# Performance work log

Measured on AMD Instinct MI355X. Metric: run time of the kernel, lower is better.

The kernel has to match this reference:

```python
import jax, jax.numpy as jnp
import numpy as np

B, N, FN, FE = 8, 256, 64, 64  # batch, nodes, node feat, edge feat


def gnn_layer(A, x, e, We, be, Wn, bn):
    # A: [B,N,N] float mask, x: [B,N,Fn], e: [B,N,N,Fe_in]
    b, n, fn = x.shape
    xi = jnp.broadcast_to(x[:, :, None, :], (b, n, n, fn))  # sender feats
    xj = jnp.broadcast_to(x[:, None, :, :], (b, n, n, fn))  # receiver feats
    h = jnp.concatenate([xi, xj, e], axis=-1)               # [B,N,N,2Fn+Fe]
    e_new = jax.nn.relu(jnp.einsum('bijk,kf->bijf', h, We) + be) * A[..., None]
    deg = jnp.clip(jnp.sum(A, axis=2), 1.0, None)           # [B,N]
    agg = jnp.sum(e_new, axis=2) / deg[..., None]           # mean over neighbors
    x_new = jax.nn.relu(jnp.concatenate([x, agg], axis=-1) @ Wn + bn)
    return x_new, e_new


def setup_inputs() -> dict:
    key = jax.random.key(0)
    ks = jax.random.split(key, 20)
    s = 0.05
    inp = {
        'edge_index': jax.random.randint(ks[0], (B, N, N), 0, 2, dtype=jnp.int32),
        'x': jax.random.normal(ks[1], (B, N, FN), dtype=jnp.float32),
        'edge_attr': jax.random.normal(ks[2], (B, N, N, FE), dtype=jnp.float32),
    }
    # 3 GNN layers: edge-update MLP (2Fn+Fe -> Fe) and node-update (Fn+Fe -> Fn)
    for l in range(3):
        inp[f'We{l}'] = jax.random.normal(ks[3 + 4 * l], (2 * FN + FE, FE), jnp.float32) * s
        inp[f'be{l}'] = jnp.zeros((FE,), jnp.float32)
        inp[f'Wn{l}'] = jax.random.normal(ks[4 + 4 * l], (FN + FE, FN), jnp.float32) * s
        inp[f'bn{l}'] = jnp.zeros((FN,), jnp.float32)
    # spectral-norm MLP head: Fe -> Fe -> Fe -> 1
    inp['W1'] = jax.random.normal(ks[15], (FE, FE), jnp.float32) * s
    inp['b1'] = jnp.zeros((FE,), jnp.float32)
    inp['W2'] = jax.random.normal(ks[16], (FE, FE), jnp.float32) * s
    inp['b2'] = jnp.zeros((FE,), jnp.float32)
    inp['W3'] = jax.random.normal(ks[17], (FE, 1), jnp.float32) * s
    inp['b3'] = jnp.zeros((1,), jnp.float32)
    return inp


def reference(edge_index, x, edge_attr,
              We0, be0, Wn0, bn0,
              We1, be1, Wn1, bn1,
              We2, be2, Wn2, bn2,
              W1, b1, W2, b2, W3, b3):
    A = edge_index.astype(jnp.float32)
    x = x.astype(jnp.float32)
    # layer 0 updates both nodes and edges
    x1, e = gnn_layer(A, x, edge_attr, We0, be0, Wn0, bn0)
    # middle layer(s): node output discarded (as in original forward)
    _, e = gnn_layer(A, x1, e, We1, be1, Wn1, bn1)
    # last layer
    _, edges = gnn_layer(A, x1, e, We2, be2, Wn2, bn2)
    # end == 'edge_mean'
    v = jnp.mean(edges, axis=(1, 2))  # [B, FE]
    h = jax.nn.relu(v @ W1 + b1)
    h = jax.nn.relu(h @ W2 + b2)
    out = h @ W3 + b3                  # [B, 1]
    return jnp.squeeze(out, axis=-1)   # [B]
```

## Files before the change

kernel.cpp:

```cpp
#include <hip/hip_runtime.h>

#define BB 8
#define NN 256
#define FF 64

typedef float f32x4 __attribute__((ext_vector_type(4)));
typedef short s16x8 __attribute__((ext_vector_type(8)));
typedef unsigned short u16;

#define MFMA_BF16(a, b, c) __builtin_amdgcn_mfma_f32_16x16x32_bf16(a, b, c, 0, 0, 0)

__device__ inline u16 f2bf(float x) {
    unsigned u = __float_as_uint(x);
    u += 0x7FFFu + ((u >> 16) & 1u);
    return (u16)(u >> 16);
}
__device__ inline float bf2f(u16 h) { return __uint_as_float(((unsigned)h) << 16); }

__device__ inline s16x8 cvt_a(float4 v0, float4 v1) {
    s16x8 a;
    a[0] = (short)f2bf(v0.x); a[1] = (short)f2bf(v0.y);
    a[2] = (short)f2bf(v0.z); a[3] = (short)f2bf(v0.w);
    a[4] = (short)f2bf(v1.x); a[5] = (short)f2bf(v1.y);
    a[6] = (short)f2bf(v1.z); a[7] = (short)f2bf(v1.w);
    return a;
}

__global__ __launch_bounds__(256) void wprep_kernel(
    const float* __restrict__ We0, const float* __restrict__ We1,
    const float* __restrict__ We2, u16* __restrict__ wimg)
{
    const float* src =
        (blockIdx.x == 0 ? We0 : (blockIdx.x == 1 ? We1 : We2)) + 2 * FF * FF;
    u16* hi = wimg + blockIdx.x * 8192;
    u16* lo = hi + 4096;
    for (int idx = threadIdx.x; idx < 4096; idx += 256) {
        const int f = idx >> 6, rem = idx & 63, cs = rem >> 3, j = rem & 7;
        const int k = ((cs ^ (f & 7)) << 3) | j;
        const float wv = src[k * FF + f];
        const u16 h = f2bf(wv);
        hi[idx] = h;
        lo[idx] = f2bf(wv - bf2f(h));
    }
}

__global__ __launch_bounds__(256) void pq_kernel(
    const float* __restrict__ x, const float* __restrict__ We,
    const float* __restrict__ be, float* __restrict__ P, float* __restrict__ QT,
    float* __restrict__ agg)
{
    const int rl = threadIdx.x >> 6, f = threadIdx.x & 63;
    const int r = blockIdx.x * 4 + rl;
    __shared__ float xs[4][FF];
    xs[rl][f] = x[r * FF + f];
    agg[r * FF + f] = 0.f;
    __syncthreads();
    float p = be[f], q = 0.f;
#pragma unroll
    for (int k = 0; k < FF; ++k) {
        const float xv = xs[rl][k];
        p = fmaf(xv, We[k * FF + f], p);
        q = fmaf(xv, We[(FF + k) * FF + f], q);
    }
    P[r * FF + f] = p;
    QT[((r >> 8) * FF + f) * NN + (r & 255)] = q;
}

__global__ __launch_bounds__(256, 4) void edge0_kernel(
    const float* e_in, const u16* __restrict__ whi,
    const u16* __restrict__ wlo, const float* __restrict__ P,
    const float* __restrict__ QT0, const int* __restrict__ A,
    u16* e1_out, float* __restrict__ agg)
{
    __shared__ u16 Whl[4096], Wll[4096];
    __shared__ u16 Et[8192];
    __shared__ float Al[128], Pl[64];

    const int tid = threadIdx.x;
    const int bt  = blockIdx.x;
    const int bi  = bt >> 1;
    const int b   = bi >> 8;
    const int j0  = (bt & 1) << 7;

#pragma unroll
    for (int m = 0; m < 2; ++m) {
        ((uint4*)Whl)[tid + 256 * m] = ((const uint4*)whi)[tid + 256 * m];
        ((uint4*)Wll)[tid + 256 * m] = ((const uint4*)wlo)[tid + 256 * m];
    }
    if (tid < 128) Al[tid] = (float)A[bi * NN + j0 + tid];
    if (tid < 64)  Pl[tid] = P[bi * FF + tid];

    const int w = tid >> 6, lane = tid & 63;
    const int quad = lane >> 4, l15 = lane & 15, l7 = lane & 7;
    const int e_base = 32 * w;

    const float* erow = e_in + ((size_t)bi * NN + j0) * FF;
    const int*   Arow = A + bi * NN + j0;

    int rm[2];
#pragma unroll
    for (int et = 0; et < 2; ++et) rm[et] = Arow[e_base + et * 16 + l15];

    float al[2][4];
#pragma unroll
    for (int et = 0; et < 2; ++et) {
        const int4 ai = *(const int4*)&Arow[e_base + et * 16 + quad * 4];
        al[et][0] = (float)ai.x; al[et][1] = (float)ai.y;
        al[et][2] = (float)ai.z; al[et][3] = (float)ai.w;
    }

    s16x8 afr[2][2];
#pragma unroll
    for (int et = 0; et < 2; ++et) {
        if (rm[et]) {
#pragma unroll
            for (int ks = 0; ks < 2; ++ks) {
                const float* p =
                    erow + (e_base + et * 16 + l15) * FF + ks * 32 + quad * 8;
                afr[ks][et] = cvt_a(*(const float4*)p, *(const float4*)(p + 4));
            }
        } else {
#pragma unroll
            for (int ks = 0; ks < 2; ++ks) afr[ks][et] = (s16x8){0,0,0,0,0,0,0,0};
        }
    }

    float qv[2][4][4];
    {
        const float* QTb = QT0 + (size_t)b * FF * NN;
#pragma unroll
        for (int et = 0; et < 2; ++et)
#pragma unroll
            for (int ft = 0; ft < 4; ++ft) {
                const float4 t = *(const float4*)
                    &QTb[(ft * 16 + l15) * NN + j0 + e_base + et * 16 + quad * 4];
                qv[et][ft][0] = t.x; qv[et][ft][1] = t.y;
                qv[et][ft][2] = t.z; qv[et][ft][3] = t.w;
            }
    }

    __syncthreads();

    f32x4 acc[2][4];
#pragma unroll
    for (int et = 0; et < 2; ++et)
#pragma unroll
        for (int ft = 0; ft < 4; ++ft) acc[et][ft] = (f32x4){0.f, 0.f, 0.f, 0.f};

#pragma unroll
    for (int ks = 0; ks < 2; ++ks)
#pragma unroll
        for (int ft = 0; ft < 4; ++ft) {
            const int f  = ft * 16 + l15;
            const int ca = (ks * 4 + quad) ^ l7;
            const s16x8 bh = *(const s16x8*)&Whl[f * 64 + ca * 8];
            const s16x8 bl = *(const s16x8*)&Wll[f * 64 + ca * 8];
#pragma unroll
            for (int et = 0; et < 2; ++et) {
                acc[et][ft] = MFMA_BF16(afr[ks][et], bh, acc[et][ft]);
                acc[et][ft] = MFMA_BF16(afr[ks][et], bl, acc[et][ft]);
            }
        }

    float psum[4] = {0.f, 0.f, 0.f, 0.f};
#pragma unroll
    for (int et = 0; et < 2; ++et)
#pragma unroll
        for (int ft = 0; ft < 4; ++ft)
#pragma unroll
            for (int r = 0; r < 4; ++r) {
                const int el = e_base + et * 16 + quad * 4 + r;
                const int f  = ft * 16 + l15;
                const float val = acc[et][ft][r] + Pl[f] + qv[et][ft][r];
                const float rv  = fmaxf(val, 0.f) * al[et][r];
                Et[el * 64 + f] = f2bf(rv);
                psum[ft] += rv;
            }
#pragma unroll
    for (int ft = 0; ft < 4; ++ft) {
        psum[ft] += __shfl_down(psum[ft], 32);
        psum[ft] += __shfl_down(psum[ft], 16);
    }
    if (lane < 16) {
#pragma unroll
        for (int ft = 0; ft < 4; ++ft)
            atomicAdd(&agg[bi * FF + ft * 16 + l15], psum[ft]);
    }

    __syncthreads();

    u16* dst = e1_out + (size_t)bt * 16384;
#pragma unroll
    for (int m = 0; m < 4; ++m) {
        const int idx = tid + 256 * m;
        const int row = idx >> 3;
        if (Al[row] != 0.f)
            ((uint4*)dst)[idx] = ((const uint4*)Et)[idx];
    }
}

__global__ __launch_bounds__(256) void nodepq_kernel(
    const float* __restrict__ x, const float* __restrict__ agg,
    const int* __restrict__ A,
    const float* __restrict__ Wn, const float* __restrict__ bn,
    const float* __restrict__ We1, const float* __restrict__ be1,
    const float* __restrict__ We2, const float* __restrict__ be2,
    float* __restrict__ P1, float* __restrict__ QT1,
    float* __restrict__ P2, float* __restrict__ QT2, float* __restrict__ v)
{
    const int rl = threadIdx.x >> 6, f = threadIdx.x & 63;
    const int r = blockIdx.x * 4 + rl;
    __shared__ float s[4][2 * FF];
    __shared__ float x1s[4][FF];

    float da = (float)A[r * NN + f] + (float)A[r * NN + f + 64] +
               (float)A[r * NN + f + 128] + (float)A[r * NN + f + 192];
#pragma unroll
    for (int off = 32; off > 0; off >>= 1) da += __shfl_down(da, off, 64);
    const float deg = fmaxf(__shfl(da, 0, 64), 1.0f);

    s[rl][f]      = x[r * FF + f];
    s[rl][FF + f] = agg[r * FF + f] / deg;
    if (blockIdx.x == 0) {
        v[threadIdx.x] = 0.f;
        v[256 + threadIdx.x] = 0.f;
    }
    __syncthreads();
    float a = bn[f];
#pragma unroll
    for (int k = 0; k < 2 * FF; ++k) a = fmaf(s[rl][k], Wn[k * FF + f], a);
    x1s[rl][f] = fmaxf(a, 0.f);
    __syncthreads();
    float p1 = be1[f], q1 = 0.f, p2 = be2[f], q2 = 0.f;
#pragma unroll
    for (int k = 0; k < FF; ++k) {
        const float xv = x1s[rl][k];
        p1 = fmaf(xv, We1[k * FF + f], p1);
        q1 = fmaf(xv, We1[(FF + k) * FF + f], q1);
        p2 = fmaf(xv, We2[k * FF + f], p2);
        q2 = fmaf(xv, We2[(FF + k) * FF + f], q2);
    }
    P1[r * FF + f] = p1;
    P2[r * FF + f] = p2;
    const int qt = ((r >> 8) * FF + f) * NN + (r & 255);
    QT1[qt] = q1;
    QT2[qt] = q2;
}

__global__ __launch_bounds__(256, 4) void edge12_kernel(
    const u16* __restrict__ e1,
    const u16* __restrict__ w1hi, const u16* __restrict__ w1lo,
    const u16* __restrict__ w2hi, const u16* __restrict__ w2lo,
    const float* __restrict__ P1, const float* __restrict__ QT1,
    const float* __restrict__ P2, const float* __restrict__ QT2,
    const int* __restrict__ A, float* __restrict__ v)
{
    __shared__ u16 Wh[4096], Wl[4096];
    __shared__ u16 E2[128 * 64];
    __shared__ float Pl1[64], Pl2[64], red[64];

    const int tid = threadIdx.x;
    const int bt  = blockIdx.x;
    const int bi  = bt >> 1;
    const int b   = bi >> 8;
    const int j0  = (bt & 1) << 7;

    const uint4 w2h0 = ((const uint4*)w2hi)[tid];
    const uint4 w2h1 = ((const uint4*)w2hi)[tid + 256];
    const uint4 w2l0 = ((const uint4*)w2lo)[tid];
    const uint4 w2l1 = ((const uint4*)w2lo)[tid + 256];

#pragma unroll
    for (int m = 0; m < 2; ++m) {
        ((uint4*)Wh)[tid + 256 * m] = ((const uint4*)w1hi)[tid + 256 * m];
        ((uint4*)Wl)[tid + 256 * m] = ((const uint4*)w1lo)[tid + 256 * m];
    }
    if (tid < 64) {
        Pl1[tid] = P1[bi * FF + tid];
        Pl2[tid] = P2[bi * FF + tid];
        red[tid] = 0.f;
    }

    const int w = tid >> 6, lane = tid & 63;
    const int quad = lane >> 4, l15 = lane & 15, l7 = lane & 7;
    const int e_base = 32 * w;

    const int* Arow = A + bi * NN + j0;

    int rm[2];
#pragma unroll
    for (int et = 0; et < 2; ++et) rm[et] = Arow[e_base + et * 16 + l15];

    float al[2][4];
#pragma unroll
    for (int et = 0; et < 2; ++et) {
        const int4 ai = *(const int4*)&Arow[e_base + et * 16 + quad * 4];
        al[et][0] = (float)ai.x; al[et][1] = (float)ai.y;
        al[et][2] = (float)ai.z; al[et][3] = (float)ai.w;
    }

    const u16* etile = e1 + (size_t)bt * 16384;
    s16x8 afr[2][2];
#pragma unroll
    for (int et = 0; et < 2; ++et) {
        if (rm[et]) {
#pragma unroll
            for (int ks = 0; ks < 2; ++ks)
                afr[ks][et] = *(const s16x8*)
                    &etile[(e_base + et * 16 + l15) * 64 + ks * 32 + quad * 8];
        } else {
#pragma unroll
            for (int ks = 0; ks < 2; ++ks) afr[ks][et] = (s16x8){0,0,0,0,0,0,0,0};
        }
    }

    float qv[2][4][4];
    {
        const float* QTb = QT1 + (size_t)b * FF * NN;
#pragma unroll
        for (int et = 0; et < 2; ++et)
#pragma unroll
            for (int ft = 0; ft < 4; ++ft) {
                const float4 t = *(const float4*)
                    &QTb[(ft * 16 + l15) * NN + j0 + e_base + et * 16 + quad * 4];
                qv[et][ft][0] = t.x; qv[et][ft][1] = t.y;
                qv[et][ft][2] = t.z; qv[et][ft][3] = t.w;
            }
    }

    __syncthreads();

    f32x4 acc[2][4];
#pragma unroll
    for (int et = 0; et < 2; ++et)
#pragma unroll
        for (int ft = 0; ft < 4; ++ft) acc[et][ft] = (f32x4){0.f, 0.f, 0.f, 0.f};

#pragma unroll
    for (int ks = 0; ks < 2; ++ks)
#pragma unroll
        for (int ft = 0; ft < 4; ++ft) {
            const int f  = ft * 16 + l15;
            const int ca = (ks * 4 + quad) ^ l7;
            const s16x8 bh = *(const s16x8*)&Wh[f * 64 + ca * 8];
            const s16x8 bl = *(const s16x8*)&Wl[f * 64 + ca * 8];
#pragma unroll
            for (int et = 0; et < 2; ++et) {
                acc[et][ft] = MFMA_BF16(afr[ks][et], bh, acc[et][ft]);
                acc[et][ft] = MFMA_BF16(afr[ks][et], bl, acc[et][ft]);
            }
        }

#pragma unroll
    for (int et = 0; et < 2; ++et)
#pragma unroll
        for (int ft = 0; ft < 4; ++ft)
#pragma unroll
            for (int r = 0; r < 4; ++r) {
                const int el = e_base + et * 16 + quad * 4 + r;
                const int f  = ft * 16 + l15;
                const float val = acc[et][ft][r] + Pl1[f] + qv[et][ft][r];
                const float rv  = fmaxf(val, 0.f) * al[et][r];
                const int c  = f >> 3;
                const int cs = c ^ (el & 7);
                E2[el * 64 + cs * 8 + l7] = f2bf(rv);
            }

    {
        const float* QTb = QT2 + (size_t)b * FF * NN;
#pragma unroll
        for (int et = 0; et < 2; ++et)
#pragma unroll
            for (int ft = 0; ft < 4; ++ft) {
                const float4 t = *(const float4*)
                    &QTb[(ft * 16 + l15) * NN + j0 + e_base + et * 16 + quad * 4];
                qv[et][ft][0] = t.x; qv[et][ft][1] = t.y;
                qv[et][ft][2] = t.z; qv[et][ft][3] = t.w;
            }
    }

    __syncthreads();

    ((uint4*)Wh)[tid]       = w2h0;
    ((uint4*)Wh)[tid + 256] = w2h1;
    ((uint4*)Wl)[tid]       = w2l0;
    ((uint4*)Wl)[tid + 256] = w2l1;

    __syncthreads();

#pragma unroll
    for (int et = 0; et < 2; ++et)
#pragma unroll
        for (int ft = 0; ft < 4; ++ft) acc[et][ft] = (f32x4){0.f, 0.f, 0.f, 0.f};

#pragma unroll
    for (int ks = 0; ks < 2; ++ks) {
        s16x8 a2[2];
#pragma unroll
        for (int et = 0; et < 2; ++et) {
            const int e  = e_base + et * 16 + l15;
            const int ca = (ks * 4 + quad) ^ l7;
            a2[et] = *(const s16x8*)&E2[e * 64 + ca * 8];
        }
#pragma unroll
        for (int ft = 0; ft < 4; ++ft) {
            const int f  = ft * 16 + l15;
            const int ca = (ks * 4 + quad) ^ l7;
            const s16x8 bh = *(const s16x8*)&Wh[f * 64 + ca * 8];
            const s16x8 bl = *(const s16x8*)&Wl[f * 64 + ca * 8];
#pragma unroll
            for (int et = 0; et < 2; ++et) {
                acc[et][ft] = MFMA_BF16(a2[et], bh, acc[et][ft]);
                acc[et][ft] = MFMA_BF16(a2[et], bl, acc[et][ft]);
            }
        }
    }

    float psum[4] = {0.f, 0.f, 0.f, 0.f};
#pragma unroll
    for (int et = 0; et < 2; ++et)
#pragma unroll
        for (int ft = 0; ft < 4; ++ft)
#pragma unroll
            for (int r = 0; r < 4; ++r) {
                const float val = acc[et][ft][r] + Pl2[ft * 16 + l15] + qv[et][ft][r];
                psum[ft] += fmaxf(val, 0.f) * al[et][r];
            }
#pragma unroll
    for (int ft = 0; ft < 4; ++ft) {
        psum[ft] += __shfl_down(psum[ft], 32);
        psum[ft] += __shfl_down(psum[ft], 16);
    }
    if (lane < 16) {
#pragma unroll
        for (int ft = 0; ft < 4; ++ft)
            atomicAdd(&red[ft * 16 + l15], psum[ft]);
    }
    __syncthreads();
    if (tid < 64) atomicAdd(&v[b * FF + tid], red[tid]);
}

__global__ __launch_bounds__(64) void head_kernel(
    const float* __restrict__ vsum, const float* __restrict__ W1,
    const float* __restrict__ b1, const float* __restrict__ W2,
    const float* __restrict__ b2, const float* __restrict__ W3,
    const float* __restrict__ b3, float* __restrict__ out)
{
    const int f = threadIdx.x;
    __shared__ float hv[BB][FF];
    __shared__ float h1[BB][FF];
#pragma unroll
    for (int b = 0; b < BB; ++b) hv[b][f] = vsum[b * FF + f] * (1.0f / 65536.0f);
    __syncthreads();
#pragma unroll
    for (int b = 0; b < BB; ++b) {
        float acc = b1[f];
#pragma unroll
        for (int k = 0; k < FF; ++k) acc = fmaf(hv[b][k], W1[k * FF + f], acc);
        h1[b][f] = fmaxf(acc, 0.f);
    }
    __syncthreads();
#pragma unroll
    for (int b = 0; b < BB; ++b) {
        float acc = b2[f];
#pragma unroll
        for (int k = 0; k < FF; ++k) acc = fmaf(h1[b][k], W2[k * FF + f], acc);
        hv[b][f] = fmaxf(acc, 0.f);
    }
    __syncthreads();
#pragma unroll
    for (int b = 0; b < BB; ++b) {
        float p = hv[b][f] * W3[f];
#pragma unroll
        for (int off = 32; off > 0; off >>= 1) p += __shfl_down(p, off);
        if (f == 0) out[b] = p + b3[0];
    }
}

extern "C" void kernel_launch(void* const* d_in, const int* in_sizes, int n_in,
                              void* d_out, int out_size, void* d_ws, size_t ws_size,
                              hipStream_t stream)
{
    const int*   A      = (const int*)d_in[0];
    const float* x      = (const float*)d_in[1];
    float*       e_attr = (float*)d_in[2];

    const float* We0 = (const float*)d_in[3];
    const float* be0 = (const float*)d_in[4];
    const float* Wn0 = (const float*)d_in[5];
    const float* bn0 = (const float*)d_in[6];
    const float* We1 = (const float*)d_in[7];
    const float* be1 = (const float*)d_in[8];
    const float* We2 = (const float*)d_in[11];
    const float* be2 = (const float*)d_in[12];
    const float* W1 = (const float*)d_in[15];
    const float* b1 = (const float*)d_in[16];
    const float* W2 = (const float*)d_in[17];
    const float* b2 = (const float*)d_in[18];
    const float* W3 = (const float*)d_in[19];
    const float* b3 = (const float*)d_in[20];
    float* out = (float*)d_out;
    (void)in_sizes; (void)n_in; (void)out_size; (void)ws_size;

    const int R = BB * NN;
    float* P0  = (float*)d_ws;
    float* QT0 = P0 + R * FF;
    float* P1  = QT0 + R * FF;
    float* QT1 = P1 + R * FF;
    float* P2  = QT1 + R * FF;
    float* QT2 = P2 + R * FF;
    float* agg = QT2 + R * FF;
    float* v   = agg + R * FF;
    u16*  wimg = (u16*)(v + 512);

    const int EB = 2 * R;

    wprep_kernel<<<3, 256, 0, stream>>>(We0, We1, We2, wimg);
    pq_kernel<<<R / 4, 256, 0, stream>>>(x, We0, be0, P0, QT0, agg);
    edge0_kernel<<<EB, 256, 0, stream>>>(e_attr, wimg, wimg + 4096, P0, QT0, A,
                                         (u16*)e_attr, agg);
    nodepq_kernel<<<R / 4, 256, 0, stream>>>(x, agg, A, Wn0, bn0, We1, be1,
                                             We2, be2, P1, QT1, P2, QT2, v);
    edge12_kernel<<<EB, 256, 0, stream>>>((const u16*)e_attr,
                                          wimg + 8192, wimg + 12288,
                                          wimg + 16384, wimg + 20480,
                                          P1, QT1, P2, QT2, A, v);
    head_kernel<<<1, 64, 0, stream>>>(v, W1, b1, W2, b2, W3, b3, out);
}
```

Before: 336.6 us.

## Trim edge kernels' LDS footprint and raise occupancy target to five blocks

Drops the small shared arrays for adjacency, P bias rows and the reduction buffer in both edge kernels. Bias values now live in registers, the adjacency mask is read from global memory, and the reduction buffer reuses the E2 tile once the A fragments have been hoisted into registers. With the lower per-block LDS use, launch bounds move from 4 to 5 blocks per CU to improve latency hiding. The higher occupancy target caps VGPRs per thread and could cause spills or serialize the MFMA schedule.

```diff
diff --git a/kernel.cpp b/kernel.cpp
--- a/kernel.cpp
+++ b/kernel.cpp
@@ -66,7 +66,7 @@
     QT[((r >> 8) * FF + f) * NN + (r & 255)] = q;
 }
 
-__global__ __launch_bounds__(256, 4) void edge0_kernel(
+__global__ __launch_bounds__(256, 5) void edge0_kernel(
     const float* e_in, const u16* __restrict__ whi,
     const u16* __restrict__ wlo, const float* __restrict__ P,
     const float* __restrict__ QT0, const int* __restrict__ A,
@@ -74,7 +74,6 @@
 {
     __shared__ u16 Whl[4096], Wll[4096];
     __shared__ u16 Et[8192];
-    __shared__ float Al[128], Pl[64];
 
     const int tid = threadIdx.x;
     const int bt  = blockIdx.x;
@@ -87,8 +86,6 @@
         ((uint4*)Whl)[tid + 256 * m] = ((const uint4*)whi)[tid + 256 * m];
         ((uint4*)Wll)[tid + 256 * m] = ((const uint4*)wlo)[tid + 256 * m];
     }
-    if (tid < 128) Al[tid] = (float)A[bi * NN + j0 + tid];
-    if (tid < 64)  Pl[tid] = P[bi * FF + tid];
 
     const int w = tid >> 6, lane = tid & 63;
     const int quad = lane >> 4, l15 = lane & 15, l7 = lane & 7;
@@ -108,6 +105,10 @@
         al[et][0] = (float)ai.x; al[et][1] = (float)ai.y;
         al[et][2] = (float)ai.z; al[et][3] = (float)ai.w;
     }
+
+    float pl[4];
+#pragma unroll
+    for (int ft = 0; ft < 4; ++ft) pl[ft] = P[bi * FF + ft * 16 + l15];
 
     s16x8 afr[2][2];
 #pragma unroll
@@ -171,7 +172,7 @@
             for (int r = 0; r < 4; ++r) {
                 const int el = e_base + et * 16 + quad * 4 + r;
                 const int f  = ft * 16 + l15;
-                const float val = acc[et][ft][r] + Pl[f] + qv[et][ft][r];
+                const float val = acc[et][ft][r] + pl[ft] + qv[et][ft][r];
                 const float rv  = fmaxf(val, 0.f) * al[et][r];
                 Et[el * 64 + f] = f2bf(rv);
                 psum[ft] += rv;
@@ -194,7 +195,7 @@
     for (int m = 0; m < 4; ++m) {
         const int idx = tid + 256 * m;
         const int row = idx >> 3;
-        if (Al[row] != 0.f)
+        if (Arow[row])
             ((uint4*)dst)[idx] = ((const uint4*)Et)[idx];
     }
 }
@@ -247,7 +248,7 @@
     QT2[qt] = q2;
 }
 
-__global__ __launch_bounds__(256, 4) void edge12_kernel(
+__global__ __launch_bounds__(256, 5) void edge12_kernel(
     const u16* __restrict__ e1,
     const u16* __restrict__ w1hi, const u16* __restrict__ w1lo,
     const u16* __restrict__ w2hi, const u16* __restrict__ w2lo,
@@ -257,7 +258,7 @@
 {
     __shared__ u16 Wh[4096], Wl[4096];
     __shared__ u16 E2[128 * 64];
-    __shared__ float Pl1[64], Pl2[64], red[64];
+    float* red = (float*)E2;
 
     const int tid = threadIdx.x;
     const int bt  = blockIdx.x;
@@ -275,11 +276,6 @@
         ((uint4*)Wh)[tid + 256 * m] = ((const uint4*)w1hi)[tid + 256 * m];
         ((uint4*)Wl)[tid + 256 * m] = ((const uint4*)w1lo)[tid + 256 * m];
     }
-    if (tid < 64) {
-        Pl1[tid] = P1[bi * FF + tid];
-        Pl2[tid] = P2[bi * FF + tid];
-        red[tid] = 0.f;
-    }
 
     const int w = tid >> 6, lane = tid & 63;
     const int quad = lane >> 4, l15 = lane & 15, l7 = lane & 7;
@@ -297,6 +293,13 @@
         const int4 ai = *(const int4*)&Arow[e_base + et * 16 + quad * 4];
         al[et][0] = (float)ai.x; al[et][1] = (float)ai.y;
         al[et][2] = (float)ai.z; al[et][3] = (float)ai.w;
+    }
+
+    float pl1[4], pl2[4];
+#pragma unroll
+    for (int ft = 0; ft < 4; ++ft) {
+        pl1[ft] = P1[bi * FF + ft * 16 + l15];
+        pl2[ft] = P2[bi * FF + ft * 16 + l15];
     }
 
     const u16* etile = e1 + (size_t)bt * 16384;
@@ -359,12 +362,22 @@
             for (int r = 0; r < 4; ++r) {
                 const int el = e_base + et * 16 + quad * 4 + r;
                 const int f  = ft * 16 + l15;
-                const float val = acc[et][ft][r] + Pl1[f] + qv[et][ft][r];
+                const float val = acc[et][ft][r] + pl1[ft] + qv[et][ft][r];
                 const float rv  = fmaxf(val, 0.f) * al[et][r];
                 const int c  = f >> 3;
                 const int cs = c ^ (el & 7);
                 E2[el * 64 + cs * 8 + l7] = f2bf(rv);
             }
+
+    s16x8 a2[2][2];
+#pragma unroll
+    for (int ks = 0; ks < 2; ++ks)
+#pragma unroll
+        for (int et = 0; et < 2; ++et) {
+            const int e  = e_base + et * 16 + l15;
+            const int ca = (ks * 4 + quad) ^ l7;
+            a2[ks][et] = *(const s16x8*)&E2[e * 64 + ca * 8];
+        }
 
     {
         const float* QTb = QT2 + (size_t)b * FF * NN;
@@ -385,6 +398,7 @@
     ((uint4*)Wh)[tid + 256] = w2h1;
     ((uint4*)Wl)[tid]       = w2l0;
     ((uint4*)Wl)[tid + 256] = w2l1;
+    if (tid < 64) red[tid] = 0.f;
 
     __syncthreads();
 
@@ -394,14 +408,7 @@
         for (int ft = 0; ft < 4; ++ft) acc[et][ft] = (f32x4){0.f, 0.f, 0.f, 0.f};
 
 #pragma unroll
-    for (int ks = 0; ks < 2; ++ks) {
-        s16x8 a2[2];
-#pragma unroll
-        for (int et = 0; et < 2; ++et) {
-            const int e  = e_base + et * 16 + l15;
-            const int ca = (ks * 4 + quad) ^ l7;
-            a2[et] = *(const s16x8*)&E2[e * 64 + ca * 8];
-        }
+    for (int ks = 0; ks < 2; ++ks)
 #pragma unroll
         for (int ft = 0; ft < 4; ++ft) {
             const int f  = ft * 16 + l15;
@@ -410,11 +417,10 @@
             const s16x8 bl = *(const s16x8*)&Wl[f * 64 + ca * 8];
 #pragma unroll
             for (int et = 0; et < 2; ++et) {
-                acc[et][ft] = MFMA_BF16(a2[et], bh, acc[et][ft]);
-                acc[et][ft] = MFMA_BF16(a2[et], bl, acc[et][ft]);
+                acc[et][ft] = MFMA_BF16(a2[ks][et], bh, acc[et][ft]);
+                acc[et][ft] = MFMA_BF16(a2[ks][et], bl, acc[et][ft]);
             }
         }
-    }
 
     float psum[4] = {0.f, 0.f, 0.f, 0.f};
 #pragma unroll
@@ -423,7 +429,7 @@
         for (int ft = 0; ft < 4; ++ft)
 #pragma unroll
             for (int r = 0; r < 4; ++r) {
-                const float val = acc[et][ft][r] + Pl2[ft * 16 + l15] + qv[et][ft][r];
+                const float val = acc[et][ft][r] + pl2[ft] + qv[et][ft][r];
                 psum[ft] += fmaxf(val, 0.f) * al[et][r];
             }
 #pragma unroll
```

Result: slower. 411.9 us (+22.4%).
